# Kernel optimization log

Hardware: AMD Instinct MI355X
Metric: run time of the kernel (lower is better)

The kernel has to match this reference:

```python
import jax, jax.numpy as jnp
import numpy as np

BS, SEQ, DIM, L = 32, 256, 6, 400
NH, DM, DFF, DOUT = 2, 4, 16, 32
MAXA, ILEN = SEQ // 2 + 2, 20
THR, HW = 0.001, 2


def _layernorm(x, g, b):
    m = x.mean(-1, keepdims=True)
    v = ((x - m) ** 2).mean(-1, keepdims=True)
    return (x - m) * jax.lax.rsqrt(v + 1e-5) * g + b


def _get_max(t, ws):
    # non-overlapping window peak suppression: keep only per-window argmax value
    bs, Lt = t.shape
    nwin = Lt // ws
    w = t[:, :nwin * ws].reshape(bs, nwin, ws)
    oh = jax.nn.one_hot(jnp.argmax(w, axis=2), ws, dtype=t.dtype)
    return (w * oh).reshape(bs, nwin * ws)


def reference(x, imu_mask, imu_len, conv_w, conv_b, W_b1, b_b1, W_fc, b_fc,
              Wqkv, Wo, ln1_g, ln1_b, Wf1, bf1, Wf2, bf2, ln2_g, ln2_b,
              Wout, bout, Wd1, bd1, Wd2, bd2, Wa, ba):
    bs, seq, dim, l = x.shape
    N = bs * seq
    # --- CNN encoder: valid conv1d -> relu -> 2-bin mean pool -> (N,32,2) ---
    y = jax.lax.conv_general_dilated(x.reshape(N, dim, l), conv_w, (1,), 'VALID',
                                     dimension_numbers=('NCH', 'OIH', 'NCH'))
    y = jax.nn.relu(y + conv_b[None, :, None])  # (N,32,398)
    half = y.shape[-1] // 2
    pooled = jnp.stack([y[:, :, :half].mean(-1), y[:, :, half:2 * half].mean(-1)], -1)
    cnn_flat = pooled.reshape(N, -1)  # (N,64)
    bridge_out = jax.nn.sigmoid(cnn_flat @ W_b1 + b_b1)  # (N,4)
    # --- one-step forecasting loss -> data-dependent peaks ---
    forcast_in = bridge_out.reshape(bs, seq, DM)
    shft = jnp.pad(forcast_in, ((0, 0), (1, 0), (0, 0)))[:, :-1]
    fmask = jnp.ones_like(forcast_in).at[:, 0, :].set(0.0)
    fmask = (fmask * imu_mask[:, :, 0, 0][:, :, None]).reshape(N, DM)
    forcast = shft.reshape(N, DM) @ W_fc + b_fc
    floss = jnp.mean(jnp.square(forcast * fmask - forcast_in.reshape(N, DM) * fmask), axis=1)
    floss = floss.reshape(bs, seq)
    lmask = jnp.ones_like(floss).at[:, :2].set(0.0).at[:, -2:].set(0.0)
    floss = floss * ((floss > THR) * lmask)
    sel = _get_max(floss, 2 * HW)            # (bs,seq)
    sel2 = _get_max(sel[:, HW:], 2 * HW)     # (bs,seq-4)
    sel2 = jnp.pad(sel2, ((0, 0), (HW, 0)))
    if sel.shape[1] > sel2.shape[1]:
        sel2 = jnp.pad(sel2, ((0, 0), (0, HW)))
    seg_points = sel2 > 0
    last = jnp.clip(jnp.round(imu_len.astype(jnp.float32) / seq).astype(jnp.int32), 2, seq)
    # --- merge unit-length segments (vectorized equivalent of the while-loop) ---
    pos = jnp.arange(seq)
    point = seg_points & (pos[None] < last[:, None])
    bnd_next = jnp.pad(point, ((0, 0), (0, 1)))[:, 1:] | (pos[None] + 1 == last[:, None])
    kept = point & ~bnd_next                 # a boundary survives iff next segment len > 1
    seg_id = jnp.cumsum(kept, axis=1)
    valid_t = pos[None] < last[:, None]
    same = (seg_id[:, :, None] == seg_id[:, None, :]) & valid_t[:, :, None] & valid_t[:, None, :]
    attn_mask = jnp.where(same | jnp.eye(seq, dtype=bool)[None], 0.0, -jnp.inf)[:, None]
    # --- 1-layer post-norm transformer with block-diagonal mask ---
    hb = bridge_out.reshape(seq, bs, DM).transpose(1, 0, 2)  # faithful reshape order
    qkv = jnp.einsum('bsd,cde->cbse', hb, Wqkv)
    hd = DM // NH
    q, k, v = [t.reshape(bs, seq, NH, hd) for t in qkv]
    scores = jnp.einsum('bqhd,bkhd->bhqk', q, k) / np.sqrt(hd) + attn_mask
    attn = jax.nn.softmax(scores, axis=-1)
    ao = jnp.einsum('bhqk,bkhd->bqhd', attn, v).reshape(bs, seq, DM) @ Wo
    h1 = _layernorm(hb + ao, ln1_g, ln1_b)
    ff = jax.nn.relu(h1 @ Wf1 + bf1) @ Wf2 + bf2
    h2 = _layernorm(h1 + ff, ln2_g, ln2_b)
    tr_out = h2 @ Wout + bout                # (bs,seq,32)
    # --- per-segment atom embeddings, padded to MAXA slots ---
    n_kept = kept.sum(1)
    kp = jnp.sort(jnp.where(kept, pos[None], seq), axis=1)[:, :MAXA]
    a_idx = jnp.arange(MAXA)
    ends = jnp.where(a_idx[None] < n_kept[:, None], kp, last[:, None])
    starts = jnp.concatenate([jnp.zeros((bs, 1), ends.dtype), ends[:, :-1]], axis=1)
    atom_valid = (a_idx[None] <= n_kept[:, None]).astype(x.dtype)
    emb = jnp.take_along_axis(tr_out, jnp.clip(ends - 1, 0, seq - 1)[:, :, None], axis=1)
    atom_gen = (emb.reshape(-1, DOUT) @ Wa + ba).reshape(bs, MAXA, dim, ILEN)
    atom_gen = atom_gen * atom_valid[:, :, None, None]
    # --- per-segment nearest resample to ILEN via one batched gather ---
    xf = x.transpose(0, 2, 1, 3).reshape(bs, dim, seq * l)
    in_len = (ends - starts) * l
    idx = starts[:, :, None] * l + (jnp.arange(ILEN)[None, None] * in_len[:, :, None]) // ILEN
    idx = jnp.clip(idx, 0, seq * l - 1)
    seg_interp = xf[jnp.arange(bs)[:, None, None], :, idx]  # (bs,MAXA,ILEN,dim)
    seg_interp = seg_interp.transpose(0, 1, 3, 2) * atom_valid[:, :, None, None]
    # --- imu decoder ---
    imu_gen = (jax.nn.relu(bridge_out @ Wd1 + bd1) @ Wd2 + bd2).reshape(bs, seq, dim, l)
    return jnp.concatenate([imu_gen.ravel(), atom_gen.ravel(), seg_interp.ravel(),
                            forcast.ravel(), floss.ravel()])


def setup_inputs() -> dict:
    key = jax.random.key(0)
    ks = jax.random.split(key, 20)
    f32 = jnp.float32
    nrm = lambda k, s, sc: jax.random.normal(k, s, f32) * sc
    inp = {
        'x': nrm(ks[0], (BS, SEQ, DIM, L), 1.0),
        'imu_mask': jnp.ones((BS, SEQ, 1, 1), f32),
        'imu_len': jax.random.randint(ks[1], (BS,), SEQ * SEQ // 2, SEQ * SEQ),
        'conv_w': nrm(ks[2], (32, DIM, 3), 0.24),
        'conv_b': jnp.zeros((32,), f32),
        'W_b1': nrm(ks[3], (64, DM), 0.125),
        'b_b1': jnp.zeros((DM,), f32),
        'W_fc': nrm(ks[4], (DM, DM), 0.5),
        'b_fc': jnp.zeros((DM,), f32),
        'Wqkv': nrm(ks[5], (3, DM, DM), 0.5),
        'Wo': nrm(ks[6], (DM, DM), 0.5),
        'ln1_g': jnp.ones((DM,), f32), 'ln1_b': jnp.zeros((DM,), f32),
        'Wf1': nrm(ks[7], (DM, DFF), 0.5), 'bf1': jnp.zeros((DFF,), f32),
        'Wf2': nrm(ks[8], (DFF, DM), 0.25), 'bf2': jnp.zeros((DM,), f32),
        'ln2_g': jnp.ones((DM,), f32), 'ln2_b': jnp.zeros((DM,), f32),
        'Wout': nrm(ks[9], (DM, DOUT), 0.5), 'bout': jnp.zeros((DOUT,), f32),
        'Wd1': nrm(ks[10], (DM, 64), 0.5), 'bd1': jnp.zeros((64,), f32),
        'Wd2': nrm(ks[11], (64, DIM * L), 0.125), 'bd2': jnp.zeros((DIM * L,), f32),
        'Wa': nrm(ks[12], (DOUT, DIM * ILEN), 0.18), 'ba': jnp.zeros((DIM * ILEN,), f32),
    }
    return inp
```

## Files before the change

kernel.cpp:

```cpp
#include <hip/hip_runtime.h>
#include <math.h>

#define OFF_IMU  0
#define OFF_ATOM 19660800
#define OFF_SEG  20160000
#define OFF_FC   20659200
#define OFF_FL   20691968

#define WS_BRIDGE 0
#define WS_TR     32768
#define WS_ENDS   303104
#define WS_STARTS 307264
#define WS_NK     311424

static __device__ __forceinline__ int imin(int a, int b) { return a < b ? a : b; }
static __device__ __forceinline__ int imax(int a, int b) { return a > b ? a : b; }

#define PK_FMA_LO(S, W, X) \
    asm("v_pk_fma_f32 %0, %1, %2, %0 op_sel:[0,0,0] op_sel_hi:[1,0,1]" \
        : "+v"(S) : "v"(W), "v"(X))
#define PK_FMA_HI(S, W, X) \
    asm("v_pk_fma_f32 %0, %1, %2, %0 op_sel:[0,1,0] op_sel_hi:[1,1,1]" \
        : "+v"(S) : "v"(W), "v"(X))

union F4 { float4 q; float2 h[2]; };

__global__ __launch_bounds__(128) void k1_conv_bridge(
    const float* __restrict__ x, const float* __restrict__ conv_w,
    const float* __restrict__ conv_b, const float* __restrict__ W_b1,
    const float* __restrict__ b_b1, float* __restrict__ bridge)
{
    __shared__ __align__(16) float xs[2][2424];
    __shared__ float pooledL[2][64];
    const int tid = threadIdx.x;
    const int n0 = blockIdx.x * 2;

    const int wv = tid >> 6;
    const int l  = tid & 63;
    const int pr = l & 15;
    const int hg = (l >> 4) & 1;
    const int q  = l >> 5;

    float2 W2[18];
    {
        const float* wa = conv_w + (2 * pr) * 18;
        const float* wb = wa + 18;
#pragma unroll
        for (int j = 0; j < 18; ++j) W2[j] = make_float2(wa[j], wb[j]);
    }
    const float2 cb2 = make_float2(conv_b[2 * pr], conv_b[2 * pr + 1]);

    {
        const float4* xw = (const float4*)(x + (size_t)(n0 + wv) * 2400);
        float* xd = xs[wv];
#pragma unroll
        for (int k = 0; k < 10; ++k) {
            const int i = l + k * 64;
            if (k < 9 || i < 600) {
                const float4 v = xw[i];
                const int ic = i / 100;
                const int t4 = (i - ic * 100) * 4;
                *(float4*)&xd[ic * 404 + t4] = v;
            }
        }
        if (l < 24) xd[(l >> 2) * 404 + 400 + (l & 3)] = 0.0f;
    }

    const float* rb = &xs[wv][hg * 200 + q * 100];
    float2 accMain = make_float2(0.0f, 0.0f);
    float2 extra   = make_float2(0.0f, 0.0f);

    float2 c01[6], c23[6];
#pragma unroll
    for (int ic = 0; ic < 6; ++ic) {
        const F4 f = *(const F4*)(rb + ic * 404);
        c01[ic] = f.h[0]; c23[ic] = f.h[1];
    }

    for (int g = 0; g < 4; ++g) {
#pragma unroll
        for (int u = 0; u < 6; ++u) {
            float2 S0 = cb2, S1 = cb2, S2 = cb2, S3 = cb2;
#pragma unroll
            for (int ic = 0; ic < 6; ++ic) {
                const F4 nf = *(const F4*)(rb + ic * 404 + (u + 1) * 4);
                const float2 n01 = nf.h[0];
                const float2 w0 = W2[ic*3+0], w1 = W2[ic*3+1], w2 = W2[ic*3+2];
                PK_FMA_LO(S0, w0, c01[ic]); PK_FMA_HI(S0, w1, c01[ic]); PK_FMA_LO(S0, w2, c23[ic]);
                PK_FMA_HI(S1, w0, c01[ic]); PK_FMA_LO(S1, w1, c23[ic]); PK_FMA_HI(S1, w2, c23[ic]);
                PK_FMA_LO(S2, w0, c23[ic]); PK_FMA_HI(S2, w1, c23[ic]); PK_FMA_LO(S2, w2, n01);
                PK_FMA_HI(S3, w0, c23[ic]); PK_FMA_LO(S3, w1, n01);     PK_FMA_HI(S3, w2, n01);
                c01[ic] = n01; c23[ic] = nf.h[1];
            }
            accMain.x += fmaxf(S0.x,0.f)+fmaxf(S1.x,0.f)+fmaxf(S2.x,0.f)+fmaxf(S3.x,0.f);
            accMain.y += fmaxf(S0.y,0.f)+fmaxf(S1.y,0.f)+fmaxf(S2.y,0.f)+fmaxf(S3.y,0.f);
        }
        rb += 24;
    }

    {
        float2 S0 = cb2, S1 = cb2, S2 = cb2, S3 = cb2;
#pragma unroll
        for (int ic = 0; ic < 6; ++ic) {
            const F4 nf = *(const F4*)(rb + ic * 404 + 4);
            const float2 n01 = nf.h[0];
            const float2 w0 = W2[ic*3+0], w1 = W2[ic*3+1], w2 = W2[ic*3+2];
            PK_FMA_LO(S0, w0, c01[ic]); PK_FMA_HI(S0, w1, c01[ic]); PK_FMA_LO(S0, w2, c23[ic]);
            PK_FMA_HI(S1, w0, c01[ic]); PK_FMA_LO(S1, w1, c23[ic]); PK_FMA_HI(S1, w2, c23[ic]);
            PK_FMA_LO(S2, w0, c23[ic]); PK_FMA_HI(S2, w1, c23[ic]); PK_FMA_LO(S2, w2, n01);
            PK_FMA_HI(S3, w0, c23[ic]); PK_FMA_LO(S3, w1, n01);     PK_FMA_HI(S3, w2, n01);
        }
        const float r0x = fmaxf(S0.x,0.f), r0y = fmaxf(S0.y,0.f);
        const float r1x = fmaxf(S1.x,0.f), r1y = fmaxf(S1.y,0.f);
        const float r2x = fmaxf(S2.x,0.f), r2y = fmaxf(S2.y,0.f);
        const float r3x = fmaxf(S3.x,0.f), r3y = fmaxf(S3.y,0.f);
        if (q == 0) {
            accMain.x += r0x + r1x + r2x + r3x;
            accMain.y += r0y + r1y + r2y + r3y;
        } else if (hg == 0) {
            accMain.x += r0x + r1x + r2x;  extra.x = r3x;
            accMain.y += r0y + r1y + r2y;  extra.y = r3y;
        } else {
            accMain.x += r0x + r1x;
            accMain.y += r0y + r1y;
        }
    }

    float2 tot;
    tot.x = accMain.x + __shfl_xor(accMain.x, 32);
    tot.y = accMain.y + __shfl_xor(accMain.y, 32);
    const float exx = __shfl_xor(extra.x, 16);
    const float exy = __shfl_xor(extra.y, 16);
    if (hg) { tot.x += exx; tot.y += exy; }
    if (q) {
        pooledL[wv][(2 * pr + 0) * 2 + hg] = tot.x * (1.0f / 199.0f);
        pooledL[wv][(2 * pr + 1) * 2 + hg] = tot.y * (1.0f / 199.0f);
    }

    {
        const float v = pooledL[wv][l];
        const float4 wb = *(const float4*)(W_b1 + l * 4);
        float p0 = v * wb.x, p1 = v * wb.y, p2 = v * wb.z, p3 = v * wb.w;
#pragma unroll
        for (int off = 1; off < 64; off <<= 1) {
            p0 += __shfl_xor(p0, off, 64);
            p1 += __shfl_xor(p1, off, 64);
            p2 += __shfl_xor(p2, off, 64);
            p3 += __shfl_xor(p3, off, 64);
        }
        if (l == 0) {
            float* bp = bridge + (size_t)(n0 + wv) * 4;
            bp[0] = 1.0f / (1.0f + __expf(-(p0 + b_b1[0])));
            bp[1] = 1.0f / (1.0f + __expf(-(p1 + b_b1[1])));
            bp[2] = 1.0f / (1.0f + __expf(-(p2 + b_b1[2])));
            bp[3] = 1.0f / (1.0f + __expf(-(p3 + b_b1[3])));
        }
    }
}

__global__ __launch_bounds__(256) void k234_seg_attn(
    const float* __restrict__ bridge, const float* __restrict__ imu_mask,
    const float* __restrict__ W_fc, const float* __restrict__ b_fc,
    const int* __restrict__ imu_len, float* __restrict__ out,
    int* __restrict__ ends_ws, int* __restrict__ starts_ws, int* __restrict__ nk_ws,
    const float* __restrict__ Wqkv, const float* __restrict__ Wo,
    const float* __restrict__ ln1_g, const float* __restrict__ ln1_b,
    const float* __restrict__ Wf1, const float* __restrict__ bf1,
    const float* __restrict__ Wf2, const float* __restrict__ bf2,
    const float* __restrict__ ln2_g, const float* __restrict__ ln2_b,
    const float* __restrict__ Wout, const float* __restrict__ bout,
    float* __restrict__ tr_ws)
{
    const int b = blockIdx.x >> 3;
    const int chunk = blockIdx.x & 7;
    const int tid = threadIdx.x;
    __shared__ float kv[256][8];
    __shared__ int sid[256];
    __shared__ float part[32][8][8];
    __shared__ float fl[256];
    __shared__ float sel[256];
    __shared__ float sp[256];
    __shared__ int pk[256];
    __shared__ int sc[2][256];
    __shared__ int kpl[256];

    {
        const float4 h = *(const float4*)(bridge + (size_t)(tid * 32 + b) * 4);
#pragma unroll
        for (int e = 0; e < 4; ++e) {
            kv[tid][e]     = h.x * Wqkv[16 + e] + h.y * Wqkv[20 + e] + h.z * Wqkv[24 + e] + h.w * Wqkv[28 + e];
            kv[tid][4 + e] = h.x * Wqkv[32 + e] + h.y * Wqkv[36 + e] + h.z * Wqkv[40 + e] + h.w * Wqkv[44 + e];
        }
    }

    {
        const int n = b * 256 + tid;
        float sh[4], cur[4];
#pragma unroll
        for (int j = 0; j < 4; ++j) {
            sh[j] = (tid == 0) ? 0.0f : bridge[(n - 1) * 4 + j];
            cur[j] = bridge[n * 4 + j];
        }
        const float fm = ((tid == 0) ? 0.0f : 1.0f) * imu_mask[n];
        float flv = 0.0f;
#pragma unroll
        for (int j = 0; j < 4; ++j) {
            float f = b_fc[j];
#pragma unroll
            for (int i = 0; i < 4; ++i) f = fmaf(sh[i], W_fc[i * 4 + j], f);
            out[OFF_FC + n * 4 + j] = f;
            const float d = (f - cur[j]) * fm;
            flv = fmaf(d, d, flv);
        }
        flv *= 0.25f;
        const bool lm = (tid >= 2) && (tid < 254);
        flv = (flv > 0.001f && lm) ? flv : 0.0f;
        out[OFF_FL + n] = flv;
        fl[tid] = flv;
        sp[tid] = 0.0f;
    }
    __syncthreads();

    if (tid < 64) {
        const int base = tid * 4;
        float m = fl[base]; int idx = 0;
#pragma unroll
        for (int i = 1; i < 4; ++i) { float v = fl[base + i]; if (v > m) { m = v; idx = i; } }
#pragma unroll
        for (int i = 0; i < 4; ++i) sel[base + i] = (i == idx) ? m : 0.0f;
    }
    __syncthreads();
    if (tid < 63) {
        const int base = 2 + tid * 4;
        float m = sel[base]; int idx = 0;
#pragma unroll
        for (int i = 1; i < 4; ++i) { float v = sel[base + i]; if (v > m) { m = v; idx = i; } }
        sp[base + idx] = (m > 0.0f) ? 1.0f : 0.0f;
    }
    __syncthreads();
    int last = (int)rintf((float)imu_len[b] * (1.0f / 256.0f));
    last = imin(imax(last, 2), 256);
    const int point = ((sp[tid] > 0.0f) && (tid < last)) ? 1 : 0;
    pk[tid] = point;
    __syncthreads();
    const int pnext = (tid < 255) ? pk[tid + 1] : 0;
    const int bnd = pnext | ((tid + 1 == last) ? 1 : 0);
    const int kept = (point && !bnd) ? 1 : 0;
    __syncthreads();
    sc[0][tid] = kept;
    __syncthreads();
    int src = 0;
    for (int off = 1; off < 256; off <<= 1) {
        const int v = sc[src][tid] + ((tid >= off) ? sc[src][tid - off] : 0);
        sc[src ^ 1][tid] = v;
        __syncthreads();
        src ^= 1;
    }
    const int myid = sc[src][tid];
    sid[tid] = myid;
    const int nk = sc[src][255];
    if (kept) kpl[myid - 1] = tid;
    __syncthreads();
    if (tid < 130) {
        ends_ws[b * 130 + tid] = (tid < nk) ? kpl[tid] : last;
        starts_ws[b * 130 + tid] = (tid == 0) ? 0 : ((tid - 1 < nk) ? kpl[tid - 1] : last);
    }
    if (tid == 0) nk_ws[b] = nk;

    const int lq = tid & 31;
    const int jg = tid >> 5;
    const int sq = chunk * 32 + lq;
    {
        const float4 h = *(const float4*)(bridge + (size_t)(sq * 32 + b) * 4);
        float qv[4];
#pragma unroll
        for (int e = 0; e < 4; ++e)
            qv[e] = h.x * Wqkv[e] + h.y * Wqkv[4 + e] + h.z * Wqkv[8 + e] + h.w * Wqkv[12 + e];
        const bool vs = sq < last;
        const int ms = sid[sq];
        const float isq = 0.70710678118654752f;
        float m0 = -1e30f, l0 = 0.f, a00 = 0.f, a01 = 0.f;
        float m1 = -1e30f, l1 = 0.f, a10 = 0.f, a11 = 0.f;
#pragma unroll 4
        for (int jj = 0; jj < 32; ++jj) {
            const int j = jg * 32 + jj;
            const bool allowed = (j == sq) || (vs && (j < last) && (sid[j] == ms));
            const float sc0 = (qv[0] * kv[j][0] + qv[1] * kv[j][1]) * isq;
            const float sc1 = (qv[2] * kv[j][2] + qv[3] * kv[j][3]) * isq;
            {
                const float mn = allowed ? fmaxf(m0, sc0) : m0;
                const float c = __expf(m0 - mn);
                const float e = allowed ? __expf(sc0 - mn) : 0.0f;
                l0 = l0 * c + e; a00 = a00 * c + e * kv[j][4]; a01 = a01 * c + e * kv[j][5]; m0 = mn;
            }
            {
                const float mn = allowed ? fmaxf(m1, sc1) : m1;
                const float c = __expf(m1 - mn);
                const float e = allowed ? __expf(sc1 - mn) : 0.0f;
                l1 = l1 * c + e; a10 = a10 * c + e * kv[j][6]; a11 = a11 * c + e * kv[j][7]; m1 = mn;
            }
        }
        float* pp = part[lq][jg];
        pp[0] = m0; pp[1] = l0; pp[2] = a00; pp[3] = a01;
        pp[4] = m1; pp[5] = l1; pp[6] = a10; pp[7] = a11;
    }
    __syncthreads();
    if (tid < 32) {
        const int s = chunk * 32 + tid;
        float M0 = -1e30f, L0 = 0.f, A00 = 0.f, A01 = 0.f;
        float M1 = -1e30f, L1 = 0.f, A10 = 0.f, A11 = 0.f;
#pragma unroll
        for (int p = 0; p < 8; ++p) {
            const float* pp = part[tid][p];
            {
                const float mn = fmaxf(M0, pp[0]);
                const float c0 = __expf(M0 - mn), c1 = __expf(pp[0] - mn);
                L0 = L0 * c0 + pp[1] * c1; A00 = A00 * c0 + pp[2] * c1; A01 = A01 * c0 + pp[3] * c1; M0 = mn;
            }
            {
                const float mn = fmaxf(M1, pp[4]);
                const float c0 = __expf(M1 - mn), c1 = __expf(pp[4] - mn);
                L1 = L1 * c0 + pp[5] * c1; A10 = A10 * c0 + pp[6] * c1; A11 = A11 * c0 + pp[7] * c1; M1 = mn;
            }
        }
        const float4 h = *(const float4*)(bridge + (size_t)(s * 32 + b) * 4);
        const float hb0 = h.x, hb1 = h.y, hb2 = h.z, hb3 = h.w;
        float ao[4] = {A00 / L0, A01 / L0, A10 / L1, A11 / L1};
        float x1[4];
#pragma unroll
        for (int jj = 0; jj < 4; ++jj)
            x1[jj] = ao[0] * Wo[jj] + ao[1] * Wo[4 + jj] + ao[2] * Wo[8 + jj] + ao[3] * Wo[12 + jj];
        x1[0] += hb0; x1[1] += hb1; x1[2] += hb2; x1[3] += hb3;
        float mean = 0.25f * (x1[0] + x1[1] + x1[2] + x1[3]);
        float var = 0.f;
#pragma unroll
        for (int i = 0; i < 4; ++i) { float d = x1[i] - mean; var += d * d; }
        var *= 0.25f;
        const float rs1 = rsqrtf(var + 1e-5f);
        float h1v[4];
#pragma unroll
        for (int i = 0; i < 4; ++i) h1v[i] = (x1[i] - mean) * rs1 * ln1_g[i] + ln1_b[i];
        float o2[4] = {bf2[0], bf2[1], bf2[2], bf2[3]};
#pragma unroll
        for (int kk = 0; kk < 16; ++kk) {
            float t = bf1[kk];
#pragma unroll
            for (int i = 0; i < 4; ++i) t = fmaf(h1v[i], Wf1[i * 16 + kk], t);
            t = fmaxf(t, 0.0f);
#pragma unroll
            for (int jj = 0; jj < 4; ++jj) o2[jj] = fmaf(t, Wf2[kk * 4 + jj], o2[jj]);
        }
        float x2[4];
#pragma unroll
        for (int i = 0; i < 4; ++i) x2[i] = h1v[i] + o2[i];
        float mean2 = 0.25f * (x2[0] + x2[1] + x2[2] + x2[3]);
        float var2 = 0.f;
#pragma unroll
        for (int i = 0; i < 4; ++i) { float d = x2[i] - mean2; var2 += d * d; }
        var2 *= 0.25f;
        const float rs2 = rsqrtf(var2 + 1e-5f);
        float h2v[4];
#pragma unroll
        for (int i = 0; i < 4; ++i) h2v[i] = (x2[i] - mean2) * rs2 * ln2_g[i] + ln2_b[i];
        float* tp = tr_ws + ((size_t)(b * 256 + s)) * 32;
#pragma unroll
        for (int mm = 0; mm < 32; ++mm)
            tp[mm] = bout[mm] + h2v[0] * Wout[mm] + h2v[1] * Wout[32 + mm]
                   + h2v[2] * Wout[64 + mm] + h2v[3] * Wout[96 + mm];
    }
}

__global__ __launch_bounds__(128) void k5_atoms(
    const float* __restrict__ x, const float* __restrict__ tr_ws,
    const int* __restrict__ ends_ws, const int* __restrict__ starts_ws,
    const int* __restrict__ nk_ws,
    const float* __restrict__ Wa, const float* __restrict__ ba,
    float* __restrict__ out)
{
    const int a = blockIdx.x;
    const int b = blockIdx.y;
    const int tid = threadIdx.x;
    __shared__ float emb[32];
    const int e = ends_ws[b * 130 + a];
    const int st = starts_ws[b * 130 + a];
    const int nk = nk_ws[b];
    const float valid = (a <= nk) ? 1.0f : 0.0f;
    const int ec = imin(imax(e - 1, 0), 255);
    if (tid < 32) emb[tid] = tr_ws[((size_t)(b * 256 + ec)) * 32 + tid];
    __syncthreads();
    if (tid < 120) {
        float v = ba[tid];
#pragma unroll
        for (int f = 0; f < 32; ++f) v = fmaf(emb[f], Wa[f * 120 + tid], v);
        out[OFF_ATOM + ((size_t)(b * 130 + a)) * 120 + tid] = v * valid;
        const int d = tid / 20, i = tid % 20;
        const int ilen = (e - st) * 400;
        int idx = st * 400 + (i * ilen) / 20;
        idx = imin(imax(idx, 0), 102399);
        const int si = idx / 400, ti = idx % 400;
        const float px = x[(((size_t)b * 256 + si) * 6 + d) * 400 + ti];
        out[OFF_SEG + ((size_t)(b * 130 + a)) * 120 + tid] = px * valid;
    }
}

__global__ __launch_bounds__(256) void k6_imu(
    const float* __restrict__ bridge, const float* __restrict__ Wd1,
    const float* __restrict__ bd1, const float* __restrict__ Wd2,
    const float* __restrict__ bd2, float* __restrict__ out)
{
    __shared__ float hl[64 * 32];
    const int n0 = blockIdx.x * 32;
    const int mb = blockIdx.y;
    const int tid = threadIdx.x;
    for (int e = tid; e < 2048; e += 256) {
        const int f = e >> 5, i = e & 31;
        const float4 br = *(const float4*)(bridge + (size_t)(n0 + i) * 4);
        const float v = bd1[f] + br.x * Wd1[f] + br.y * Wd1[64 + f]
                      + br.z * Wd1[128 + f] + br.w * Wd1[192 + f];
        hl[f * 32 + i] = fmaxf(v, 0.0f);
    }
    __syncthreads();
    const int gm = tid & 63, gn = tid >> 6;
    const int m0 = mb * 256 + gm * 4;
    if (m0 >= 2400) return;
    float acc[8][4];
#pragma unroll
    for (int r = 0; r < 8; ++r)
#pragma unroll
        for (int c = 0; c < 4; ++c) acc[r][c] = 0.f;
#pragma unroll 4
    for (int f = 0; f < 64; ++f) {
        const float4 w4 = *(const float4*)&Wd2[(size_t)f * 2400 + m0];
        const float4 h0 = *(const float4*)&hl[f * 32 + gn * 8];
        const float4 h1 = *(const float4*)&hl[f * 32 + gn * 8 + 4];
        const float hv[8] = {h0.x, h0.y, h0.z, h0.w, h1.x, h1.y, h1.z, h1.w};
        const float wv[4] = {w4.x, w4.y, w4.z, w4.w};
#pragma unroll
        for (int r = 0; r < 8; ++r)
#pragma unroll
            for (int c = 0; c < 4; ++c) acc[r][c] = fmaf(hv[r], wv[c], acc[r][c]);
    }
    const float4 bb = *(const float4*)&bd2[m0];
#pragma unroll
    for (int r = 0; r < 8; ++r) {
        float4 o;
        o.x = acc[r][0] + bb.x; o.y = acc[r][1] + bb.y;
        o.z = acc[r][2] + bb.z; o.w = acc[r][3] + bb.w;
        *(float4*)&out[OFF_IMU + (size_t)(n0 + gn * 8 + r) * 2400 + m0] = o;
    }
}

extern "C" void kernel_launch(void* const* d_in, const int* in_sizes, int n_in,
                              void* d_out, int out_size, void* d_ws, size_t ws_size,
                              hipStream_t stream)
{
    const float* x        = (const float*)d_in[0];
    const float* imu_mask = (const float*)d_in[1];
    const int*   imu_len  = (const int*)  d_in[2];
    const float* conv_w   = (const float*)d_in[3];
    const float* conv_b   = (const float*)d_in[4];
    const float* W_b1     = (const float*)d_in[5];
    const float* b_b1     = (const float*)d_in[6];
    const float* W_fc     = (const float*)d_in[7];
    const float* b_fc     = (const float*)d_in[8];
    const float* Wqkv     = (const float*)d_in[9];
    const float* Wo       = (const float*)d_in[10];
    const float* ln1_g    = (const float*)d_in[11];
    const float* ln1_b    = (const float*)d_in[12];
    const float* Wf1      = (const float*)d_in[13];
    const float* bf1      = (const float*)d_in[14];
    const float* Wf2      = (const float*)d_in[15];
    const float* bf2      = (const float*)d_in[16];
    const float* ln2_g    = (const float*)d_in[17];
    const float* ln2_b    = (const float*)d_in[18];
    const float* Wout     = (const float*)d_in[19];
    const float* bout     = (const float*)d_in[20];
    const float* Wd1      = (const float*)d_in[21];
    const float* bd1      = (const float*)d_in[22];
    const float* Wd2      = (const float*)d_in[23];
    const float* bd2      = (const float*)d_in[24];
    const float* Wa       = (const float*)d_in[25];
    const float* ba       = (const float*)d_in[26];

    float* out = (float*)d_out;
    float* wsf = (float*)d_ws;
    int*   wsi = (int*)d_ws;

    float* bridge = wsf + WS_BRIDGE;
    float* tr_ws  = wsf + WS_TR;
    int* ends   = wsi + WS_ENDS;
    int* starts = wsi + WS_STARTS;
    int* nk     = wsi + WS_NK;

    k1_conv_bridge<<<4096, 128, 0, stream>>>(x, conv_w, conv_b, W_b1, b_b1, bridge);
    k234_seg_attn<<<256, 256, 0, stream>>>(bridge, imu_mask, W_fc, b_fc, imu_len,
                                           out, ends, starts, nk,
                                           Wqkv, Wo, ln1_g, ln1_b, Wf1, bf1,
                                           Wf2, bf2, ln2_g, ln2_b, Wout, bout, tr_ws);
    k5_atoms<<<dim3(130, 32), 128, 0, stream>>>(x, tr_ws, ends, starts, nk, Wa, ba, out);
    k6_imu<<<dim3(256, 10), 256, 0, stream>>>(bridge, Wd1, bd1, Wd2, bd2, out);
}
```

Baseline: 114.8 us.

## Compute conv1d on MFMA with split bf16 hi/lo emulating fp32 precision

Replaces the packed-FMA scalar convolution with an implicit-GEMM formulation on 16x16x32 bf16 MFMA instructions. Inputs and weights are split into hi and lo bf16 parts, and three MFMA products (hi*hi, hi*lo, lo*hi) approximate fp32 accuracy. Input staging in shared memory now stores the packed hi/lo pairs, and the pooling reduction is rewritten to match the MFMA output layout. This shifts the conv FLOPs onto matrix cores. The cost is extra conversion work, gather-style LDS reads with perm shuffles, and slightly reduced precision.

New measurement: 112.5 us. -2.0%, faster.

```diff
diff --git a/kernel.cpp b/kernel.cpp
--- a/kernel.cpp
+++ b/kernel.cpp
@@ -1,4 +1,5 @@
 #include <hip/hip_runtime.h>
+#include <hip/hip_bf16.h>
 #include <math.h>
 
 #define OFF_IMU  0
@@ -16,43 +17,38 @@
 static __device__ __forceinline__ int imin(int a, int b) { return a < b ? a : b; }
 static __device__ __forceinline__ int imax(int a, int b) { return a > b ? a : b; }
 
-#define PK_FMA_LO(S, W, X) \
-    asm("v_pk_fma_f32 %0, %1, %2, %0 op_sel:[0,0,0] op_sel_hi:[1,0,1]" \
-        : "+v"(S) : "v"(W), "v"(X))
-#define PK_FMA_HI(S, W, X) \
-    asm("v_pk_fma_f32 %0, %1, %2, %0 op_sel:[0,1,0] op_sel_hi:[1,1,1]" \
-        : "+v"(S) : "v"(W), "v"(X))
-
-union F4 { float4 q; float2 h[2]; };
+typedef __attribute__((ext_vector_type(8))) short bf16x8;
+typedef __attribute__((ext_vector_type(4))) float f32x4;
+union AF { uint32_t u[4]; bf16x8 v; };
+
+static __device__ __forceinline__ uint32_t pack_hilo(float x)
+{
+    __hip_bfloat16 h = __float2bfloat16(x);
+    const float hf = __bfloat162float(h);
+    __hip_bfloat16 lo = __float2bfloat16(x - hf);
+    const uint32_t hb = *(const unsigned short*)&h;
+    const uint32_t lb = *(const unsigned short*)&lo;
+    return hb | (lb << 16);
+}
 
 __global__ __launch_bounds__(128) void k1_conv_bridge(
     const float* __restrict__ x, const float* __restrict__ conv_w,
     const float* __restrict__ conv_b, const float* __restrict__ W_b1,
     const float* __restrict__ b_b1, float* __restrict__ bridge)
 {
-    __shared__ __align__(16) float xs[2][2424];
+    __shared__ __align__(16) uint32_t xsu[2][2424];
     __shared__ float pooledL[2][64];
     const int tid = threadIdx.x;
     const int n0 = blockIdx.x * 2;
 
     const int wv = tid >> 6;
     const int l  = tid & 63;
-    const int pr = l & 15;
-    const int hg = (l >> 4) & 1;
-    const int q  = l >> 5;
-
-    float2 W2[18];
-    {
-        const float* wa = conv_w + (2 * pr) * 18;
-        const float* wb = wa + 18;
-#pragma unroll
-        for (int j = 0; j < 18; ++j) W2[j] = make_float2(wa[j], wb[j]);
-    }
-    const float2 cb2 = make_float2(conv_b[2 * pr], conv_b[2 * pr + 1]);
+    const int r  = l & 15;
+    const int kb = l >> 4;
 
     {
         const float4* xw = (const float4*)(x + (size_t)(n0 + wv) * 2400);
-        float* xd = xs[wv];
+        uint32_t* xd = xsu[wv];
 #pragma unroll
         for (int k = 0; k < 10; ++k) {
             const int i = l + k * 64;
@@ -60,100 +56,105 @@
                 const float4 v = xw[i];
                 const int ic = i / 100;
                 const int t4 = (i - ic * 100) * 4;
-                *(float4*)&xd[ic * 404 + t4] = v;
+                uint4 p;
+                p.x = pack_hilo(v.x); p.y = pack_hilo(v.y);
+                p.z = pack_hilo(v.z); p.w = pack_hilo(v.w);
+                *(uint4*)&xd[ic * 404 + t4] = p;
             }
         }
-        if (l < 24) xd[(l >> 2) * 404 + 400 + (l & 3)] = 0.0f;
-    }
-
-    const float* rb = &xs[wv][hg * 200 + q * 100];
-    float2 accMain = make_float2(0.0f, 0.0f);
-    float2 extra   = make_float2(0.0f, 0.0f);
-
-    float2 c01[6], c23[6];
-#pragma unroll
-    for (int ic = 0; ic < 6; ++ic) {
-        const F4 f = *(const F4*)(rb + ic * 404);
-        c01[ic] = f.h[0]; c23[ic] = f.h[1];
-    }
-
-    for (int g = 0; g < 4; ++g) {
-#pragma unroll
-        for (int u = 0; u < 6; ++u) {
-            float2 S0 = cb2, S1 = cb2, S2 = cb2, S3 = cb2;
-#pragma unroll
-            for (int ic = 0; ic < 6; ++ic) {
-                const F4 nf = *(const F4*)(rb + ic * 404 + (u + 1) * 4);
-                const float2 n01 = nf.h[0];
-                const float2 w0 = W2[ic*3+0], w1 = W2[ic*3+1], w2 = W2[ic*3+2];
-                PK_FMA_LO(S0, w0, c01[ic]); PK_FMA_HI(S0, w1, c01[ic]); PK_FMA_LO(S0, w2, c23[ic]);
-                PK_FMA_HI(S1, w0, c01[ic]); PK_FMA_LO(S1, w1, c23[ic]); PK_FMA_HI(S1, w2, c23[ic]);
-                PK_FMA_LO(S2, w0, c23[ic]); PK_FMA_HI(S2, w1, c23[ic]); PK_FMA_LO(S2, w2, n01);
-                PK_FMA_HI(S3, w0, c23[ic]); PK_FMA_LO(S3, w1, n01);     PK_FMA_HI(S3, w2, n01);
-                c01[ic] = n01; c23[ic] = nf.h[1];
-            }
-            accMain.x += fmaxf(S0.x,0.f)+fmaxf(S1.x,0.f)+fmaxf(S2.x,0.f)+fmaxf(S3.x,0.f);
-            accMain.y += fmaxf(S0.y,0.f)+fmaxf(S1.y,0.f)+fmaxf(S2.y,0.f)+fmaxf(S3.y,0.f);
-        }
-        rb += 24;
-    }
-
-    {
-        float2 S0 = cb2, S1 = cb2, S2 = cb2, S3 = cb2;
-#pragma unroll
-        for (int ic = 0; ic < 6; ++ic) {
-            const F4 nf = *(const F4*)(rb + ic * 404 + 4);
-            const float2 n01 = nf.h[0];
-            const float2 w0 = W2[ic*3+0], w1 = W2[ic*3+1], w2 = W2[ic*3+2];
-            PK_FMA_LO(S0, w0, c01[ic]); PK_FMA_HI(S0, w1, c01[ic]); PK_FMA_LO(S0, w2, c23[ic]);
-            PK_FMA_HI(S1, w0, c01[ic]); PK_FMA_LO(S1, w1, c23[ic]); PK_FMA_HI(S1, w2, c23[ic]);
-            PK_FMA_LO(S2, w0, c23[ic]); PK_FMA_HI(S2, w1, c23[ic]); PK_FMA_LO(S2, w2, n01);
-            PK_FMA_HI(S3, w0, c23[ic]); PK_FMA_LO(S3, w1, n01);     PK_FMA_HI(S3, w2, n01);
-        }
-        const float r0x = fmaxf(S0.x,0.f), r0y = fmaxf(S0.y,0.f);
-        const float r1x = fmaxf(S1.x,0.f), r1y = fmaxf(S1.y,0.f);
-        const float r2x = fmaxf(S2.x,0.f), r2y = fmaxf(S2.y,0.f);
-        const float r3x = fmaxf(S3.x,0.f), r3y = fmaxf(S3.y,0.f);
-        if (q == 0) {
-            accMain.x += r0x + r1x + r2x + r3x;
-            accMain.y += r0y + r1y + r2y + r3y;
-        } else if (hg == 0) {
-            accMain.x += r0x + r1x + r2x;  extra.x = r3x;
-            accMain.y += r0y + r1y + r2y;  extra.y = r3y;
-        } else {
-            accMain.x += r0x + r1x;
-            accMain.y += r0y + r1y;
-        }
-    }
-
-    float2 tot;
-    tot.x = accMain.x + __shfl_xor(accMain.x, 32);
-    tot.y = accMain.y + __shfl_xor(accMain.y, 32);
-    const float exx = __shfl_xor(extra.x, 16);
-    const float exy = __shfl_xor(extra.y, 16);
-    if (hg) { tot.x += exx; tot.y += exy; }
-    if (q) {
-        pooledL[wv][(2 * pr + 0) * 2 + hg] = tot.x * (1.0f / 199.0f);
-        pooledL[wv][(2 * pr + 1) * 2 + hg] = tot.y * (1.0f / 199.0f);
+        if (l < 24) xd[(l >> 2) * 404 + 400 + (l & 3)] = 0;
+    }
+
+    AF Bhi[2], Blo[2];
+    float bias[2];
+#pragma unroll
+    for (int ot = 0; ot < 2; ++ot) {
+        const float* wp = conv_w + (size_t)(r + ot * 16) * 18;
+#pragma unroll
+        for (int j = 0; j < 4; ++j) {
+            const int k0 = kb * 8 + 2 * j, k1 = k0 + 1;
+            const float w0 = (k0 < 18) ? wp[k0] : 0.0f;
+            const float w1 = (k1 < 18) ? wp[k1] : 0.0f;
+            const uint32_t e0 = pack_hilo(w0), e1 = pack_hilo(w1);
+            Bhi[ot].u[j] = (e0 & 0xffffu) | (e1 << 16);
+            Blo[ot].u[j] = (e0 >> 16) | (e1 & 0xffff0000u);
+        }
+        bias[ot] = conv_b[r + ot * 16];
+    }
+
+    int eoff[8];
+#pragma unroll
+    for (int s = 0; s < 8; ++s) {
+        const int k = kb * 8 + s;
+        const int ic = k / 3;
+        const int dt = k - 3 * ic;
+        eoff[s] = (k < 18) ? (ic * 404 + dt) : 0;
+    }
+    const uint32_t* ab = xsu[wv] + r;
+
+    float p00 = 0.f, p01 = 0.f, p10 = 0.f, p11 = 0.f;
+
+#pragma unroll
+    for (int tile = 0; tile < 25; ++tile) {
+        uint32_t e[8];
+#pragma unroll
+        for (int s = 0; s < 8; ++s) e[s] = ab[eoff[s] + tile * 16];
+        AF Ahi, Alo;
+#pragma unroll
+        for (int j = 0; j < 4; ++j) {
+            Ahi.u[j] = __builtin_amdgcn_perm(e[2 * j + 1], e[2 * j], 0x05040100u);
+            Alo.u[j] = __builtin_amdgcn_perm(e[2 * j + 1], e[2 * j], 0x07060302u);
+        }
+        f32x4 acc0 = {0.f, 0.f, 0.f, 0.f};
+        f32x4 acc1 = {0.f, 0.f, 0.f, 0.f};
+        acc0 = __builtin_amdgcn_mfma_f32_16x16x32_bf16(Ahi.v, Bhi[0].v, acc0, 0, 0, 0);
+        acc1 = __builtin_amdgcn_mfma_f32_16x16x32_bf16(Ahi.v, Bhi[1].v, acc1, 0, 0, 0);
+        acc0 = __builtin_amdgcn_mfma_f32_16x16x32_bf16(Ahi.v, Blo[0].v, acc0, 0, 0, 0);
+        acc1 = __builtin_amdgcn_mfma_f32_16x16x32_bf16(Ahi.v, Blo[1].v, acc1, 0, 0, 0);
+        acc0 = __builtin_amdgcn_mfma_f32_16x16x32_bf16(Alo.v, Bhi[0].v, acc0, 0, 0, 0);
+        acc1 = __builtin_amdgcn_mfma_f32_16x16x32_bf16(Alo.v, Bhi[1].v, acc1, 0, 0, 0);
+#pragma unroll
+        for (int reg = 0; reg < 4; ++reg) {
+            const int t = tile * 16 + kb * 4 + reg;
+            const float r0 = fmaxf(acc0[reg] + bias[0], 0.0f);
+            const float r1 = fmaxf(acc1[reg] + bias[1], 0.0f);
+            const bool h0 = t < 199;
+            const bool h1 = (t >= 199) && (t < 398);
+            p00 += h0 ? r0 : 0.0f;  p01 += h1 ? r0 : 0.0f;
+            p10 += h0 ? r1 : 0.0f;  p11 += h1 ? r1 : 0.0f;
+        }
+    }
+
+    p00 += __shfl_xor(p00, 16); p00 += __shfl_xor(p00, 32);
+    p01 += __shfl_xor(p01, 16); p01 += __shfl_xor(p01, 32);
+    p10 += __shfl_xor(p10, 16); p10 += __shfl_xor(p10, 32);
+    p11 += __shfl_xor(p11, 16); p11 += __shfl_xor(p11, 32);
+
+    const float inv199 = 1.0f / 199.0f;
+    if (l < 16) {
+        pooledL[wv][l * 2 + 0] = p00 * inv199;
+        pooledL[wv][l * 2 + 1] = p01 * inv199;
+        pooledL[wv][(l + 16) * 2 + 0] = p10 * inv199;
+        pooledL[wv][(l + 16) * 2 + 1] = p11 * inv199;
     }
 
     {
         const float v = pooledL[wv][l];
         const float4 wb = *(const float4*)(W_b1 + l * 4);
-        float p0 = v * wb.x, p1 = v * wb.y, p2 = v * wb.z, p3 = v * wb.w;
+        float q0 = v * wb.x, q1 = v * wb.y, q2 = v * wb.z, q3 = v * wb.w;
 #pragma unroll
         for (int off = 1; off < 64; off <<= 1) {
-            p0 += __shfl_xor(p0, off, 64);
-            p1 += __shfl_xor(p1, off, 64);
-            p2 += __shfl_xor(p2, off, 64);
-            p3 += __shfl_xor(p3, off, 64);
+            q0 += __shfl_xor(q0, off, 64);
+            q1 += __shfl_xor(q1, off, 64);
+            q2 += __shfl_xor(q2, off, 64);
+            q3 += __shfl_xor(q3, off, 64);
         }
         if (l == 0) {
             float* bp = bridge + (size_t)(n0 + wv) * 4;
-            bp[0] = 1.0f / (1.0f + __expf(-(p0 + b_b1[0])));
-            bp[1] = 1.0f / (1.0f + __expf(-(p1 + b_b1[1])));
-            bp[2] = 1.0f / (1.0f + __expf(-(p2 + b_b1[2])));
-            bp[3] = 1.0f / (1.0f + __expf(-(p3 + b_b1[3])));
+            bp[0] = 1.0f / (1.0f + __expf(-(q0 + b_b1[0])));
+            bp[1] = 1.0f / (1.0f + __expf(-(q1 + b_b1[1])));
+            bp[2] = 1.0f / (1.0f + __expf(-(q2 + b_b1[2])));
+            bp[3] = 1.0f / (1.0f + __expf(-(q3 + b_b1[3])));
         }
     }
 }
```

## Merge IMU decoder blocks into attention kernel launch as extra blocks

Applied to the files above, without the earlier changes.

The separate k6_imu kernel is folded into the segmentation/attention kernel. Blocks with index 256 and above run the decoder GEMM, and a union-style shared memory buffer serves both roles. The small attention grid (256 blocks) can now run alongside the 2560 decoder blocks, and one launch plus one inter-kernel gap is removed. In exchange, the decoder blocks now use the larger attention shared-memory footprint and register allocation, which may lower their occupancy.

After: 104.2 us (median of 2 runs). 9.3% less time.

```diff
diff --git a/kernel.cpp b/kernel.cpp
--- a/kernel.cpp
+++ b/kernel.cpp
@@ -158,7 +158,20 @@
     }
 }
 
-__global__ __launch_bounds__(256) void k234_seg_attn(
+struct S234 {
+    float kv[256][8];
+    int   sid[256];
+    float part[32][8][8];
+    float fl[256];
+    float sel[256];
+    float sp[256];
+    int   pk[256];
+    int   sc[2][256];
+    int   kpl[256];
+};
+struct S6 { float hl[64 * 32]; };
+
+__global__ __launch_bounds__(256) void k2346_attn_imu(
     const float* __restrict__ bridge, const float* __restrict__ imu_mask,
     const float* __restrict__ W_fc, const float* __restrict__ b_fc,
     const int* __restrict__ imu_len, float* __restrict__ out,
@@ -169,27 +182,67 @@
     const float* __restrict__ Wf2, const float* __restrict__ bf2,
     const float* __restrict__ ln2_g, const float* __restrict__ ln2_b,
     const float* __restrict__ Wout, const float* __restrict__ bout,
-    float* __restrict__ tr_ws)
+    float* __restrict__ tr_ws,
+    const float* __restrict__ Wd1, const float* __restrict__ bd1,
+    const float* __restrict__ Wd2, const float* __restrict__ bd2)
 {
+    __shared__ __align__(16) char smem[sizeof(S234)];
+    const int tid = threadIdx.x;
+
+    if (blockIdx.x >= 256) {
+        S6& sm = *(S6*)smem;
+        const int bx = blockIdx.x - 256;
+        const int n0 = (bx & 255) * 32;
+        const int mb = bx >> 8;
+        for (int e = tid; e < 2048; e += 256) {
+            const int f = e >> 5, i = e & 31;
+            const float4 br = *(const float4*)(bridge + (size_t)(n0 + i) * 4);
+            const float v = bd1[f] + br.x * Wd1[f] + br.y * Wd1[64 + f]
+                          + br.z * Wd1[128 + f] + br.w * Wd1[192 + f];
+            sm.hl[f * 32 + i] = fmaxf(v, 0.0f);
+        }
+        __syncthreads();
+        const int gm = tid & 63, gn = tid >> 6;
+        const int m0 = mb * 256 + gm * 4;
+        if (m0 >= 2400) return;
+        float acc[8][4];
+#pragma unroll
+        for (int r = 0; r < 8; ++r)
+#pragma unroll
+            for (int c = 0; c < 4; ++c) acc[r][c] = 0.f;
+#pragma unroll 4
+        for (int f = 0; f < 64; ++f) {
+            const float4 w4 = *(const float4*)&Wd2[(size_t)f * 2400 + m0];
+            const float4 h0 = *(const float4*)&sm.hl[f * 32 + gn * 8];
+            const float4 h1 = *(const float4*)&sm.hl[f * 32 + gn * 8 + 4];
+            const float hv[8] = {h0.x, h0.y, h0.z, h0.w, h1.x, h1.y, h1.z, h1.w};
+            const float wv[4] = {w4.x, w4.y, w4.z, w4.w};
+#pragma unroll
+            for (int r = 0; r < 8; ++r)
+#pragma unroll
+                for (int c = 0; c < 4; ++c) acc[r][c] = fmaf(hv[r], wv[c], acc[r][c]);
+        }
+        const float4 bb = *(const float4*)&bd2[m0];
+#pragma unroll
+        for (int r = 0; r < 8; ++r) {
+            float4 o;
+            o.x = acc[r][0] + bb.x; o.y = acc[r][1] + bb.y;
+            o.z = acc[r][2] + bb.z; o.w = acc[r][3] + bb.w;
+            *(float4*)&out[OFF_IMU + (size_t)(n0 + gn * 8 + r) * 2400 + m0] = o;
+        }
+        return;
+    }
+
+    S234& sm = *(S234*)smem;
     const int b = blockIdx.x >> 3;
     const int chunk = blockIdx.x & 7;
-    const int tid = threadIdx.x;
-    __shared__ float kv[256][8];
-    __shared__ int sid[256];
-    __shared__ float part[32][8][8];
-    __shared__ float fl[256];
-    __shared__ float sel[256];
-    __shared__ float sp[256];
-    __shared__ int pk[256];
-    __shared__ int sc[2][256];
-    __shared__ int kpl[256];
 
     {
         const float4 h = *(const float4*)(bridge + (size_t)(tid * 32 + b) * 4);
 #pragma unroll
         for (int e = 0; e < 4; ++e) {
-            kv[tid][e]     = h.x * Wqkv[16 + e] + h.y * Wqkv[20 + e] + h.z * Wqkv[24 + e] + h.w * Wqkv[28 + e];
-            kv[tid][4 + e] = h.x * Wqkv[32 + e] + h.y * Wqkv[36 + e] + h.z * Wqkv[40 + e] + h.w * Wqkv[44 + e];
+            sm.kv[tid][e]     = h.x * Wqkv[16 + e] + h.y * Wqkv[20 + e] + h.z * Wqkv[24 + e] + h.w * Wqkv[28 + e];
+            sm.kv[tid][4 + e] = h.x * Wqkv[32 + e] + h.y * Wqkv[36 + e] + h.z * Wqkv[40 + e] + h.w * Wqkv[44 + e];
         }
     }
 
@@ -216,54 +269,54 @@
         const bool lm = (tid >= 2) && (tid < 254);
         flv = (flv > 0.001f && lm) ? flv : 0.0f;
         out[OFF_FL + n] = flv;
-        fl[tid] = flv;
-        sp[tid] = 0.0f;
+        sm.fl[tid] = flv;
+        sm.sp[tid] = 0.0f;
     }
     __syncthreads();
 
     if (tid < 64) {
         const int base = tid * 4;
-        float m = fl[base]; int idx = 0;
-#pragma unroll
-        for (int i = 1; i < 4; ++i) { float v = fl[base + i]; if (v > m) { m = v; idx = i; } }
-#pragma unroll
-        for (int i = 0; i < 4; ++i) sel[base + i] = (i == idx) ? m : 0.0f;
+        float m = sm.fl[base]; int idx = 0;
+#pragma unroll
+        for (int i = 1; i < 4; ++i) { float v = sm.fl[base + i]; if (v > m) { m = v; idx = i; } }
+#pragma unroll
+        for (int i = 0; i < 4; ++i) sm.sel[base + i] = (i == idx) ? m : 0.0f;
     }
     __syncthreads();
     if (tid < 63) {
         const int base = 2 + tid * 4;
-        float m = sel[base]; int idx = 0;
-#pragma unroll
-        for (int i = 1; i < 4; ++i) { float v = sel[base + i]; if (v > m) { m = v; idx = i; } }
-        sp[base + idx] = (m > 0.0f) ? 1.0f : 0.0f;
+        float m = sm.sel[base]; int idx = 0;
+#pragma unroll
+        for (int i = 1; i < 4; ++i) { float v = sm.sel[base + i]; if (v > m) { m = v; idx = i; } }
+        sm.sp[base + idx] = (m > 0.0f) ? 1.0f : 0.0f;
     }
     __syncthreads();
     int last = (int)rintf((float)imu_len[b] * (1.0f / 256.0f));
     last = imin(imax(last, 2), 256);
-    const int point = ((sp[tid] > 0.0f) && (tid < last)) ? 1 : 0;
-    pk[tid] = point;
-    __syncthreads();
-    const int pnext = (tid < 255) ? pk[tid + 1] : 0;
+    const int point = ((sm.sp[tid] > 0.0f) && (tid < last)) ? 1 : 0;
+    sm.pk[tid] = point;
+    __syncthreads();
+    const int pnext = (tid < 255) ? sm.pk[tid + 1] : 0;
     const int bnd = pnext | ((tid + 1 == last) ? 1 : 0);
     const int kept = (point && !bnd) ? 1 : 0;
     __syncthreads();
-    sc[0][tid] = kept;
+    sm.sc[0][tid] = kept;
     __syncthreads();
     int src = 0;
     for (int off = 1; off < 256; off <<= 1) {
-        const int v = sc[src][tid] + ((tid >= off) ? sc[src][tid - off] : 0);
-        sc[src ^ 1][tid] = v;
+        const int v = sm.sc[src][tid] + ((tid >= off) ? sm.sc[src][tid - off] : 0);
+        sm.sc[src ^ 1][tid] = v;
         __syncthreads();
         src ^= 1;
     }
-    const int myid = sc[src][tid];
-    sid[tid] = myid;
-    const int nk = sc[src][255];
-    if (kept) kpl[myid - 1] = tid;
+    const int myid = sm.sc[src][tid];
+    sm.sid[tid] = myid;
+    const int nk = sm.sc[src][255];
+    if (kept) sm.kpl[myid - 1] = tid;
     __syncthreads();
     if (tid < 130) {
-        ends_ws[b * 130 + tid] = (tid < nk) ? kpl[tid] : last;
-        starts_ws[b * 130 + tid] = (tid == 0) ? 0 : ((tid - 1 < nk) ? kpl[tid - 1] : last);
+        ends_ws[b * 130 + tid] = (tid < nk) ? sm.kpl[tid] : last;
+        starts_ws[b * 130 + tid] = (tid == 0) ? 0 : ((tid - 1 < nk) ? sm.kpl[tid - 1] : last);
     }
     if (tid == 0) nk_ws[b] = nk;
 
@@ -277,30 +330,30 @@
         for (int e = 0; e < 4; ++e)
             qv[e] = h.x * Wqkv[e] + h.y * Wqkv[4 + e] + h.z * Wqkv[8 + e] + h.w * Wqkv[12 + e];
         const bool vs = sq < last;
-        const int ms = sid[sq];
+        const int ms = sm.sid[sq];
         const float isq = 0.70710678118654752f;
         float m0 = -1e30f, l0 = 0.f, a00 = 0.f, a01 = 0.f;
         float m1 = -1e30f, l1 = 0.f, a10 = 0.f, a11 = 0.f;
 #pragma unroll 4
         for (int jj = 0; jj < 32; ++jj) {
             const int j = jg * 32 + jj;
-            const bool allowed = (j == sq) || (vs && (j < last) && (sid[j] == ms));
-            const float sc0 = (qv[0] * kv[j][0] + qv[1] * kv[j][1]) * isq;
-            const float sc1 = (qv[2] * kv[j][2] + qv[3] * kv[j][3]) * isq;
+            const bool allowed = (j == sq) || (vs && (j < last) && (sm.sid[j] == ms));
+            const float sc0 = (qv[0] * sm.kv[j][0] + qv[1] * sm.kv[j][1]) * isq;
+            const float sc1 = (qv[2] * sm.kv[j][2] + qv[3] * sm.kv[j][3]) * isq;
             {
                 const float mn = allowed ? fmaxf(m0, sc0) : m0;
                 const float c = __expf(m0 - mn);
                 const float e = allowed ? __expf(sc0 - mn) : 0.0f;
-                l0 = l0 * c + e; a00 = a00 * c + e * kv[j][4]; a01 = a01 * c + e * kv[j][5]; m0 = mn;
+                l0 = l0 * c + e; a00 = a00 * c + e * sm.kv[j][4]; a01 = a01 * c + e * sm.kv[j][5]; m0 = mn;
             }
             {
                 const float mn = allowed ? fmaxf(m1, sc1) : m1;
                 const float c = __expf(m1 - mn);
                 const float e = allowed ? __expf(sc1 - mn) : 0.0f;
-                l1 = l1 * c + e; a10 = a10 * c + e * kv[j][6]; a11 = a11 * c + e * kv[j][7]; m1 = mn;
+                l1 = l1 * c + e; a10 = a10 * c + e * sm.kv[j][6]; a11 = a11 * c + e * sm.kv[j][7]; m1 = mn;
             }
         }
-        float* pp = part[lq][jg];
+        float* pp = sm.part[lq][jg];
         pp[0] = m0; pp[1] = l0; pp[2] = a00; pp[3] = a01;
         pp[4] = m1; pp[5] = l1; pp[6] = a10; pp[7] = a11;
     }
@@ -311,7 +364,7 @@
         float M1 = -1e30f, L1 = 0.f, A10 = 0.f, A11 = 0.f;
 #pragma unroll
         for (int p = 0; p < 8; ++p) {
-            const float* pp = part[tid][p];
+            const float* pp = sm.part[tid][p];
             {
                 const float mn = fmaxf(M0, pp[0]);
                 const float c0 = __expf(M0 - mn), c1 = __expf(pp[0] - mn);
@@ -400,53 +453,6 @@
         const int si = idx / 400, ti = idx % 400;
         const float px = x[(((size_t)b * 256 + si) * 6 + d) * 400 + ti];
         out[OFF_SEG + ((size_t)(b * 130 + a)) * 120 + tid] = px * valid;
-    }
-}
-
-__global__ __launch_bounds__(256) void k6_imu(
-    const float* __restrict__ bridge, const float* __restrict__ Wd1,
-    const float* __restrict__ bd1, const float* __restrict__ Wd2,
-    const float* __restrict__ bd2, float* __restrict__ out)
-{
-    __shared__ float hl[64 * 32];
-    const int n0 = blockIdx.x * 32;
-    const int mb = blockIdx.y;
-    const int tid = threadIdx.x;
-    for (int e = tid; e < 2048; e += 256) {
-        const int f = e >> 5, i = e & 31;
-        const float4 br = *(const float4*)(bridge + (size_t)(n0 + i) * 4);
-        const float v = bd1[f] + br.x * Wd1[f] + br.y * Wd1[64 + f]
-                      + br.z * Wd1[128 + f] + br.w * Wd1[192 + f];
-        hl[f * 32 + i] = fmaxf(v, 0.0f);
-    }
-    __syncthreads();
-    const int gm = tid & 63, gn = tid >> 6;
-    const int m0 = mb * 256 + gm * 4;
-    if (m0 >= 2400) return;
-    float acc[8][4];
-#pragma unroll
-    for (int r = 0; r < 8; ++r)
-#pragma unroll
-        for (int c = 0; c < 4; ++c) acc[r][c] = 0.f;
-#pragma unroll 4
-    for (int f = 0; f < 64; ++f) {
-        const float4 w4 = *(const float4*)&Wd2[(size_t)f * 2400 + m0];
-        const float4 h0 = *(const float4*)&hl[f * 32 + gn * 8];
-        const float4 h1 = *(const float4*)&hl[f * 32 + gn * 8 + 4];
-        const float hv[8] = {h0.x, h0.y, h0.z, h0.w, h1.x, h1.y, h1.z, h1.w};
-        const float wv[4] = {w4.x, w4.y, w4.z, w4.w};
-#pragma unroll
-        for (int r = 0; r < 8; ++r)
-#pragma unroll
-            for (int c = 0; c < 4; ++c) acc[r][c] = fmaf(hv[r], wv[c], acc[r][c]);
-    }
-    const float4 bb = *(const float4*)&bd2[m0];
-#pragma unroll
-    for (int r = 0; r < 8; ++r) {
-        float4 o;
-        o.x = acc[r][0] + bb.x; o.y = acc[r][1] + bb.y;
-        o.z = acc[r][2] + bb.z; o.w = acc[r][3] + bb.w;
-        *(float4*)&out[OFF_IMU + (size_t)(n0 + gn * 8 + r) * 2400 + m0] = o;
     }
 }
 
@@ -493,10 +499,10 @@
     int* nk     = wsi + WS_NK;
 
     k1_conv_bridge<<<4096, 128, 0, stream>>>(x, conv_w, conv_b, W_b1, b_b1, bridge);
-    k234_seg_attn<<<256, 256, 0, stream>>>(bridge, imu_mask, W_fc, b_fc, imu_len,
-                                           out, ends, starts, nk,
-                                           Wqkv, Wo, ln1_g, ln1_b, Wf1, bf1,
-                                           Wf2, bf2, ln2_g, ln2_b, Wout, bout, tr_ws);
+    k2346_attn_imu<<<2816, 256, 0, stream>>>(bridge, imu_mask, W_fc, b_fc, imu_len,
+                                             out, ends, starts, nk,
+                                             Wqkv, Wo, ln1_g, ln1_b, Wf1, bf1,
+                                             Wf2, bf2, ln2_g, ln2_b, Wout, bout,
+                                             tr_ws, Wd1, bd1, Wd2, bd2);
     k5_atoms<<<dim3(130, 32), 128, 0, stream>>>(x, tr_ws, ends, starts, nk, Wa, ba, out);
-    k6_imu<<<dim3(256, 10), 256, 0, stream>>>(bridge, Wd1, bd1, Wd2, bd2, out);
 }
```
